# Optimization experiments

Hardware: AMD Instinct MI355X
Metric: run time of the kernel (lower is better)

## Reference

```python
import jax, jax.numpy as jnp
import numpy as np

D_MODEL = 1024
N_HEADS = 16
D_K = D_MODEL // N_HEADS
SCALE = float(np.sqrt(D_K))


def setup_inputs() -> dict:
    key = jax.random.key(0)
    ks = jax.random.split(key, 11)
    B, L, D = 2, 2048, D_MODEL
    s = 1.0 / np.sqrt(D)
    inp = {
        "q": jax.random.normal(ks[0], (B, L, D), dtype=jnp.float32),
        "k": jax.random.normal(ks[1], (B, L, D), dtype=jnp.float32),
        "v": jax.random.normal(ks[2], (B, L, D), dtype=jnp.float32),
        "Wq": jax.random.normal(ks[3], (D, D), dtype=jnp.float32) * s,
        "bq": jnp.zeros((D,), dtype=jnp.float32),
        "Wk": jax.random.normal(ks[4], (D, D), dtype=jnp.float32) * s,
        "bk": jnp.zeros((D,), dtype=jnp.float32),
        "Wv": jax.random.normal(ks[5], (D, D), dtype=jnp.float32) * s,
        "bv": jnp.zeros((D,), dtype=jnp.float32),
        "Wo": jax.random.normal(ks[6], (D, D), dtype=jnp.float32) * s,
        "bo": jnp.zeros((D,), dtype=jnp.float32),
    }
    return inp


def reference(q, k, v, Wq, bq, Wk, bk, Wv, bv, Wo, bo):
    B, L, D = q.shape
    H, Dk = N_HEADS, D_K
    # projections: [B,L,D] -> [B,H,L,Dk]
    def proj(x, W, b):
        y = x @ W + b
        return y.reshape(B, -1, H, Dk).transpose(0, 2, 1, 3)
    qh = proj(q, Wq, bq)
    kh = proj(k, Wk, bk)
    vh = proj(v, Wv, bv)
    # scores [B,H,Lq,Lk]
    scores = jnp.einsum("bhqd,bhkd->bhqk", qh, kh) / SCALE
    attn = jax.nn.softmax(scores, axis=-1)  # dropout=0.0 -> identity
    out = jnp.einsum("bhqk,bhkd->bhqd", attn, vh)
    out = out.transpose(0, 2, 1, 3).reshape(B, -1, D)
    return out @ Wo + bo
```

## Files before the change

### kernel.cpp

```cpp
#include <hip/hip_runtime.h>
#include <hip/hip_bf16.h>
#include <stdint.h>
#include <stddef.h>

typedef unsigned short ushortT;
typedef __attribute__((ext_vector_type(8))) short bf16x8s;
typedef __attribute__((ext_vector_type(4))) float f32x4;


__device__ __forceinline__ short f2bf(float f) {
  unsigned u = __float_as_uint(f);
  u += 0x7FFFu + ((u >> 16) & 1u);
  return (short)(u >> 16);
}

__device__ __forceinline__ bf16x8s cvt8(const float* src) {
  const float4* p = (const float4*)src;
  float4 a = p[0], b = p[1];
  bf16x8s r;
  r[0] = f2bf(a.x); r[1] = f2bf(a.y); r[2] = f2bf(a.z); r[3] = f2bf(a.w);
  r[4] = f2bf(b.x); r[5] = f2bf(b.y); r[6] = f2bf(b.z); r[7] = f2bf(b.w);
  return r;
}

__device__ __forceinline__ void load_lds16(const ushortT* g, ushortT* l) {
  __builtin_amdgcn_global_load_lds(
      (const __attribute__((address_space(1))) void*)(g),
      (__attribute__((address_space(3))) void*)(l), 16, 0, 0);
}

__global__ __launch_bounds__(256)
void prep(const float* __restrict__ q, const float* __restrict__ k,
          const float* __restrict__ v,
          const float* __restrict__ Wq, const float* __restrict__ Wk,
          const float* __restrict__ Wv, const float* __restrict__ Wo,
          ushortT* __restrict__ Qc, ushortT* __restrict__ Kc,
          ushortT* __restrict__ Vc, ushortT* __restrict__ Wt)
{
  const int z = blockIdx.z;
  if (z < 4) {
    if (blockIdx.x >= 1024) return;
    __shared__ __align__(16) ushortT t[32][33];
    const float* W = (z == 0) ? Wq : (z == 1) ? Wk : (z == 2) ? Wv : Wo;
    ushortT* dst = Wt + (size_t)z * 1024 * 1024;
    const int x = (blockIdx.x & 31) * 32, y = (blockIdx.x >> 5) * 32;
    const int tx = threadIdx.x & 31, ty = threadIdx.x >> 5;
#pragma unroll
    for (int i = ty; i < 32; i += 8)
      t[i][tx] = (ushortT)f2bf(W[(size_t)(y + i) * 1024 + x + tx]);
    __syncthreads();
#pragma unroll
    for (int i = ty; i < 32; i += 8)
      dst[(size_t)(x + i) * 1024 + y + tx] = t[tx][i];
  } else {
    const float* src = (z == 4) ? q : (z == 5) ? k : v;
    ushortT* dst = (z == 4) ? Qc : (z == 5) ? Kc : Vc;
    const size_t i8 = ((size_t)blockIdx.x * 256 + threadIdx.x) * 8;
    *(bf16x8s*)(dst + i8) = cvt8(src + i8);
  }
}

__device__ __forceinline__ void gemm_core_128(
    const ushortT* __restrict__ A, const ushortT* __restrict__ Bt,
    int K, ushortT* As, ushortT* Bs, f32x4 (&acc)[4][4], int m0, int n0)
{
  const int tid  = threadIdx.x;
  const int wave = tid >> 6, lane = tid & 63;
  const int wm = (wave & 1) << 6;
  const int wn = (wave >> 1) << 6;
  const int lr = lane & 15;
  const int lk = (lane >> 4) << 3;

#pragma unroll
  for (int mi = 0; mi < 4; ++mi)
#pragma unroll
    for (int ni = 0; ni < 4; ++ni)
      acc[mi][ni] = (f32x4){0.f, 0.f, 0.f, 0.f};

  for (int k0 = 0; k0 < K; k0 += 32) {
    __syncthreads();
#pragma unroll
    for (int i = 0; i < 2; ++i) {
      const int cc  = tid + (i << 8);
      const int row = cc >> 2;
      const int ko  = (cc & 3) << 3;
      load_lds16(A  + (size_t)(m0 + row) * K + k0 + ko, As + cc * 8);
      load_lds16(Bt + (size_t)(n0 + row) * K + k0 + ko, Bs + cc * 8);
    }
    __syncthreads();

    bf16x8s af[4], bfr[4];
#pragma unroll
    for (int i = 0; i < 4; ++i)
      af[i] = *(const bf16x8s*)(As + (wm + i * 16 + lr) * 32 + lk);
#pragma unroll
    for (int i = 0; i < 4; ++i)
      bfr[i] = *(const bf16x8s*)(Bs + (wn + i * 16 + lr) * 32 + lk);

#pragma unroll
    for (int mi = 0; mi < 4; ++mi)
#pragma unroll
      for (int ni = 0; ni < 4; ++ni)
        acc[mi][ni] = __builtin_amdgcn_mfma_f32_16x16x32_bf16(
            af[mi], bfr[ni], acc[mi][ni], 0, 0, 0);
  }
}

__global__ __launch_bounds__(256)
void proj_gemm(const ushortT* __restrict__ Qc, const ushortT* __restrict__ Kc,
               const ushortT* __restrict__ Vc, const ushortT* __restrict__ WtAll,
               const float* __restrict__ bq, const float* __restrict__ bk,
               const float* __restrict__ bv,
               ushortT* __restrict__ Qh, ushortT* __restrict__ Kh,
               ushortT* __restrict__ Vt)
{
  __shared__ __align__(16) ushortT As[128 * 32];
  __shared__ __align__(16) ushortT Bs[128 * 32];
  const int which = blockIdx.z;
  const ushortT* A  = (which == 0) ? Qc : (which == 1) ? Kc : Vc;
  const ushortT* Bt = WtAll + (size_t)which * 1024 * 1024;
  const float* bias = (which == 0) ? bq : (which == 1) ? bk : bv;
  const int m0 = blockIdx.x * 128, n0 = blockIdx.y * 128;

  f32x4 acc[4][4];
  gemm_core_128(A, Bt, 1024, As, Bs, acc, m0, n0);

  const int lane = threadIdx.x & 63, wave = threadIdx.x >> 6;
  const int wm = (wave & 1) << 6, wn = (wave >> 1) << 6;
  const int lr = lane & 15, quad = lane >> 4;
  const float QSCALE = 0.18033688011112042f;

#pragma unroll
  for (int ni = 0; ni < 4; ++ni) {
    const int n = n0 + wn + ni * 16 + lr;
    const float bias_v = bias[n];
    const int h = n >> 6, d = n & 63;
#pragma unroll
    for (int mi = 0; mi < 4; ++mi) {
#pragma unroll
      for (int r = 0; r < 4; ++r) {
        const int m = m0 + wm + mi * 16 + quad * 4 + r;
        const int b = m >> 11, l = m & 2047;
        float val = acc[mi][ni][r] + bias_v;
        if (which == 0) val *= QSCALE;
        const ushortT o = (ushortT)f2bf(val);
        const size_t bh = (size_t)(b * 16 + h);
        if (which == 0)      Qh[(bh * 2048 + l) * 64 + d] = o;
        else if (which == 1) Kh[(bh * 2048 + l) * 64 + d] = o;
        else                 Vt[(bh * 64 + d) * 2048 + l] = o;
      }
    }
  }
}

__global__ __launch_bounds__(256)
void attn_kernel(const ushortT* __restrict__ Qh, const ushortT* __restrict__ Kh,
                 const ushortT* __restrict__ Vt, ushortT* __restrict__ Ob)
{
  const int b = blockIdx.z, h = blockIdx.y, qt = blockIdx.x;
  const int bh = b * 16 + h;
  const int wave = threadIdx.x >> 6, lane = threadIdx.x & 63;
  const int lr = lane & 15, quad = lane >> 4, lk = quad * 8;
  const int q0 = qt * 128 + wave * 32;

  const ushortT* Q = Qh + ((size_t)bh * 2048 + q0) * 64;
  const ushortT* K = Kh + (size_t)bh * 2048 * 64;
  const ushortT* V = Vt + (size_t)bh * 64 * 2048;

  __shared__ __align__(16) ushortT Ks[64 * 76];
  __shared__ __align__(16) ushortT Vs[64 * 76];
  __shared__ __align__(16) ushortT P4[4][32 * 76];
  ushortT* Pw = P4[wave];

  bf16x8s qf[2][2];
#pragma unroll
  for (int mt = 0; mt < 2; ++mt) {
    qf[mt][0] = *(const bf16x8s*)(Q + (mt * 16 + lr) * 64 + lk);
    qf[mt][1] = *(const bf16x8s*)(Q + (mt * 16 + lr) * 64 + 32 + lk);
  }

  f32x4 o[2][4];
#pragma unroll
  for (int mt = 0; mt < 2; ++mt)
#pragma unroll
    for (int nt = 0; nt < 4; ++nt) o[mt][nt] = (f32x4){0.f, 0.f, 0.f, 0.f};
  float lsum[2][4] = {{0.f, 0.f, 0.f, 0.f}, {0.f, 0.f, 0.f, 0.f}};

  const int tid = threadIdx.x;
  const int srow = tid >> 3;
  const int sc8  = (tid & 7) << 3;

  bf16x8s kch[2], vch[2];
#pragma unroll
  for (int i = 0; i < 2; ++i) {
    const int row = srow + i * 32;
    kch[i] = *(const bf16x8s*)(K + (size_t)row * 64 + sc8);
    vch[i] = *(const bf16x8s*)(V + (size_t)row * 2048 + sc8);
  }

  for (int kt = 0; kt < 2048; kt += 64) {
    __syncthreads();
#pragma unroll
    for (int i = 0; i < 2; ++i) {
      const int row = srow + i * 32;
      *(bf16x8s*)(Ks + row * 76 + sc8) = kch[i];
      *(bf16x8s*)(Vs + row * 76 + sc8) = vch[i];
    }
    __syncthreads();

    const int kn = (kt + 64) & 2047;
#pragma unroll
    for (int i = 0; i < 2; ++i) {
      const int row = srow + i * 32;
      kch[i] = *(const bf16x8s*)(K + (size_t)(kn + row) * 64 + sc8);
      vch[i] = *(const bf16x8s*)(V + (size_t)row * 2048 + kn + sc8);
    }

    f32x4 s[2][4];
#pragma unroll
    for (int mt = 0; mt < 2; ++mt)
#pragma unroll
      for (int t = 0; t < 4; ++t) s[mt][t] = (f32x4){0.f, 0.f, 0.f, 0.f};
#pragma unroll
    for (int t = 0; t < 4; ++t) {
      const bf16x8s kf0 = *(const bf16x8s*)(Ks + (t * 16 + lr) * 76 + lk);
      const bf16x8s kf1 = *(const bf16x8s*)(Ks + (t * 16 + lr) * 76 + 32 + lk);
#pragma unroll
      for (int mt = 0; mt < 2; ++mt) {
        s[mt][t] = __builtin_amdgcn_mfma_f32_16x16x32_bf16(qf[mt][0], kf0, s[mt][t], 0, 0, 0);
        s[mt][t] = __builtin_amdgcn_mfma_f32_16x16x32_bf16(qf[mt][1], kf1, s[mt][t], 0, 0, 0);
      }
    }

#pragma unroll
    for (int mt = 0; mt < 2; ++mt)
#pragma unroll
      for (int t = 0; t < 4; ++t)
#pragma unroll
        for (int r = 0; r < 4; ++r) {
          const float p = __builtin_amdgcn_exp2f(s[mt][t][r]);
          lsum[mt][r] += p;
          Pw[(mt * 16 + quad * 4 + r) * 76 + t * 16 + lr] = (ushortT)f2bf(p);
        }
    asm volatile("s_waitcnt lgkmcnt(0)" ::: "memory");

    bf16x8s pf[2][2];
#pragma unroll
    for (int mt = 0; mt < 2; ++mt) {
      pf[mt][0] = *(const bf16x8s*)(Pw + (mt * 16 + lr) * 76 + lk);
      pf[mt][1] = *(const bf16x8s*)(Pw + (mt * 16 + lr) * 76 + 32 + lk);
    }
#pragma unroll
    for (int nt = 0; nt < 4; ++nt) {
      const bf16x8s vf0 = *(const bf16x8s*)(Vs + (nt * 16 + lr) * 76 + lk);
      const bf16x8s vf1 = *(const bf16x8s*)(Vs + (nt * 16 + lr) * 76 + 32 + lk);
#pragma unroll
      for (int mt = 0; mt < 2; ++mt) {
        o[mt][nt] = __builtin_amdgcn_mfma_f32_16x16x32_bf16(pf[mt][0], vf0, o[mt][nt], 0, 0, 0);
        o[mt][nt] = __builtin_amdgcn_mfma_f32_16x16x32_bf16(pf[mt][1], vf1, o[mt][nt], 0, 0, 0);
      }
    }
  }

  float inv[2][4];
#pragma unroll
  for (int mt = 0; mt < 2; ++mt)
#pragma unroll
    for (int r = 0; r < 4; ++r) {
      float s = lsum[mt][r];
      s += __shfl_xor(s, 1);
      s += __shfl_xor(s, 2);
      s += __shfl_xor(s, 4);
      s += __shfl_xor(s, 8);
      inv[mt][r] = 1.0f / s;
    }
#pragma unroll
  for (int mt = 0; mt < 2; ++mt)
#pragma unroll
    for (int nt = 0; nt < 4; ++nt) {
      const int dcol = h * 64 + nt * 16 + lr;
#pragma unroll
      for (int r = 0; r < 4; ++r) {
        const int l = q0 + mt * 16 + quad * 4 + r;
        Ob[((size_t)b * 2048 + l) * 1024 + dcol] =
            (ushortT)f2bf(o[mt][nt][r] * inv[mt][r]);
      }
    }
}

__global__ __launch_bounds__(256)
void out_gemm(const ushortT* __restrict__ Ob, const ushortT* __restrict__ Wto,
              const float* __restrict__ bo, float* __restrict__ C)
{
  __shared__ __align__(16) ushortT As[128 * 32];
  __shared__ __align__(16) ushortT Bs[128 * 32];
  const int m0 = blockIdx.x * 128, n0 = blockIdx.y * 128;

  f32x4 acc[4][4];
  gemm_core_128(Ob, Wto, 1024, As, Bs, acc, m0, n0);

  const int lane = threadIdx.x & 63, wave = threadIdx.x >> 6;
  const int wm = (wave & 1) << 6, wn = (wave >> 1) << 6;
  const int lr = lane & 15, quad = lane >> 4;

#pragma unroll
  for (int ni = 0; ni < 4; ++ni) {
    const int n = n0 + wn + ni * 16 + lr;
    const float bias_v = bo[n];
#pragma unroll
    for (int mi = 0; mi < 4; ++mi) {
#pragma unroll
      for (int r = 0; r < 4; ++r) {
        const int m = m0 + wm + mi * 16 + quad * 4 + r;
        C[(size_t)m * 1024 + n] = acc[mi][ni][r] + bias_v;
      }
    }
  }
}

extern "C" void kernel_launch(void* const* d_in, const int* in_sizes, int n_in,
                              void* d_out, int out_size, void* d_ws, size_t ws_size,
                              hipStream_t stream) {
  const float* q  = (const float*)d_in[0];
  const float* k  = (const float*)d_in[1];
  const float* v  = (const float*)d_in[2];
  const float* Wq = (const float*)d_in[3];
  const float* bq = (const float*)d_in[4];
  const float* Wk = (const float*)d_in[5];
  const float* bk = (const float*)d_in[6];
  const float* Wv = (const float*)d_in[7];
  const float* bv = (const float*)d_in[8];
  const float* Wo = (const float*)d_in[9];
  const float* bo = (const float*)d_in[10];

  char* ws = (char*)d_ws;
  ushortT* Wt = (ushortT*)(ws);
  ushortT* Qh = (ushortT*)(ws + (size_t)(8  << 20));
  ushortT* Kh = (ushortT*)(ws + (size_t)(16 << 20));
  ushortT* Vt = (ushortT*)(ws + (size_t)(24 << 20));
  ushortT* Qc = (ushortT*)(ws + (size_t)(32 << 20));
  ushortT* Kc = (ushortT*)(ws + (size_t)(40 << 20));
  ushortT* Vc = (ushortT*)(ws + (size_t)(48 << 20));
  ushortT* Ob = Qc;

  prep<<<dim3(2048, 1, 7), 256, 0, stream>>>(q, k, v, Wq, Wk, Wv, Wo,
                                             Qc, Kc, Vc, Wt);
  proj_gemm<<<dim3(32, 8, 3), 256, 0, stream>>>(Qc, Kc, Vc, Wt, bq, bk, bv,
                                                Qh, Kh, Vt);
  attn_kernel<<<dim3(16, 16, 2), 256, 0, stream>>>(Qh, Kh, Vt, Ob);
  out_gemm<<<dim3(32, 8), 256, 0, stream>>>(Ob, Wt + (size_t)3 * 1024 * 1024,
                                            bo, (float*)d_out);
}
```

Baseline: 265.6 us.

## Transpose score MFMA so exp results pack into vectorized P stores

```diff
diff --git a/kernel.cpp b/kernel.cpp
--- a/kernel.cpp
+++ b/kernel.cpp
@@ -169,7 +169,7 @@
 
   __shared__ __align__(16) ushortT Ks[64 * 76];
   __shared__ __align__(16) ushortT Vs[64 * 76];
-  __shared__ __align__(16) ushortT P4[4][32 * 76];
+  __shared__ __align__(16) ushortT P4[4][32 * 88];
   ushortT* Pw = P4[wave];
 
   bf16x8s qf[2][2];
@@ -184,21 +184,20 @@
   for (int mt = 0; mt < 2; ++mt)
 #pragma unroll
     for (int nt = 0; nt < 4; ++nt) o[mt][nt] = (f32x4){0.f, 0.f, 0.f, 0.f};
-  float lsum[2][4] = {{0.f, 0.f, 0.f, 0.f}, {0.f, 0.f, 0.f, 0.f}};
+  float lsum[2] = {0.f, 0.f};
 
   const int tid = threadIdx.x;
   const int srow = tid >> 3;
   const int sc8  = (tid & 7) << 3;
 
-  bf16x8s kch[2], vch[2];
-#pragma unroll
-  for (int i = 0; i < 2; ++i) {
-    const int row = srow + i * 32;
-    kch[i] = *(const bf16x8s*)(K + (size_t)row * 64 + sc8);
-    vch[i] = *(const bf16x8s*)(V + (size_t)row * 2048 + sc8);
-  }
-
   for (int kt = 0; kt < 2048; kt += 64) {
+    bf16x8s kch[2], vch[2];
+#pragma unroll
+    for (int i = 0; i < 2; ++i) {
+      const int row = srow + i * 32;
+      kch[i] = *(const bf16x8s*)(K + (size_t)(kt + row) * 64 + sc8);
+      vch[i] = *(const bf16x8s*)(V + (size_t)row * 2048 + kt + sc8);
+    }
     __syncthreads();
 #pragma unroll
     for (int i = 0; i < 2; ++i) {
@@ -208,14 +207,6 @@
     }
     __syncthreads();
 
-    const int kn = (kt + 64) & 2047;
-#pragma unroll
-    for (int i = 0; i < 2; ++i) {
-      const int row = srow + i * 32;
-      kch[i] = *(const bf16x8s*)(K + (size_t)(kn + row) * 64 + sc8);
-      vch[i] = *(const bf16x8s*)(V + (size_t)row * 2048 + kn + sc8);
-    }
-
     f32x4 s[2][4];
 #pragma unroll
     for (int mt = 0; mt < 2; ++mt)
@@ -227,28 +218,36 @@
       const bf16x8s kf1 = *(const bf16x8s*)(Ks + (t * 16 + lr) * 76 + 32 + lk);
 #pragma unroll
       for (int mt = 0; mt < 2; ++mt) {
-        s[mt][t] = __builtin_amdgcn_mfma_f32_16x16x32_bf16(qf[mt][0], kf0, s[mt][t], 0, 0, 0);
-        s[mt][t] = __builtin_amdgcn_mfma_f32_16x16x32_bf16(qf[mt][1], kf1, s[mt][t], 0, 0, 0);
+        s[mt][t] = __builtin_amdgcn_mfma_f32_16x16x32_bf16(kf0, qf[mt][0], s[mt][t], 0, 0, 0);
+        s[mt][t] = __builtin_amdgcn_mfma_f32_16x16x32_bf16(kf1, qf[mt][1], s[mt][t], 0, 0, 0);
       }
     }
 
 #pragma unroll
     for (int mt = 0; mt < 2; ++mt)
 #pragma unroll
-      for (int t = 0; t < 4; ++t)
-#pragma unroll
-        for (int r = 0; r < 4; ++r) {
-          const float p = __builtin_amdgcn_exp2f(s[mt][t][r]);
-          lsum[mt][r] += p;
-          Pw[(mt * 16 + quad * 4 + r) * 76 + t * 16 + lr] = (ushortT)f2bf(p);
-        }
+      for (int t = 0; t < 4; ++t) {
+        const float e0 = __builtin_amdgcn_exp2f(s[mt][t][0]);
+        const float e1 = __builtin_amdgcn_exp2f(s[mt][t][1]);
+        const float e2 = __builtin_amdgcn_exp2f(s[mt][t][2]);
+        const float e3 = __builtin_amdgcn_exp2f(s[mt][t][3]);
+        lsum[mt] += (e0 + e1) + (e2 + e3);
+        const unsigned a0 = __float_as_uint(e0) + 0x8000u;
+        const unsigned a1 = __float_as_uint(e1) + 0x8000u;
+        const unsigned a2 = __float_as_uint(e2) + 0x8000u;
+        const unsigned a3 = __float_as_uint(e3) + 0x8000u;
+        uint2 d;
+        d.x = (a0 >> 16) | (a1 & 0xFFFF0000u);
+        d.y = (a2 >> 16) | (a3 & 0xFFFF0000u);
+        *(uint2*)(Pw + (mt * 16 + lr) * 88 + t * 16 + quad * 4) = d;
+      }
     asm volatile("s_waitcnt lgkmcnt(0)" ::: "memory");
 
     bf16x8s pf[2][2];
 #pragma unroll
     for (int mt = 0; mt < 2; ++mt) {
-      pf[mt][0] = *(const bf16x8s*)(Pw + (mt * 16 + lr) * 76 + lk);
-      pf[mt][1] = *(const bf16x8s*)(Pw + (mt * 16 + lr) * 76 + 32 + lk);
+      pf[mt][0] = *(const bf16x8s*)(Pw + (mt * 16 + lr) * 88 + lk);
+      pf[mt][1] = *(const bf16x8s*)(Pw + (mt * 16 + lr) * 88 + 32 + lk);
     }
 #pragma unroll
     for (int nt = 0; nt < 4; ++nt) {
@@ -262,18 +261,21 @@
     }
   }
 
-  float inv[2][4];
+  float* fP = (float*)Pw;
+#pragma unroll
+  for (int mt = 0; mt < 2; ++mt) {
+    float s = lsum[mt];
+    s += __shfl_xor(s, 16);
+    s += __shfl_xor(s, 32);
+    fP[mt * 16 + lr] = 1.0f / s;
+  }
+  asm volatile("s_waitcnt lgkmcnt(0)" ::: "memory");
+  float invr[2][4];
 #pragma unroll
   for (int mt = 0; mt < 2; ++mt)
 #pragma unroll
-    for (int r = 0; r < 4; ++r) {
-      float s = lsum[mt][r];
-      s += __shfl_xor(s, 1);
-      s += __shfl_xor(s, 2);
-      s += __shfl_xor(s, 4);
-      s += __shfl_xor(s, 8);
-      inv[mt][r] = 1.0f / s;
-    }
+    for (int r = 0; r < 4; ++r) invr[mt][r] = fP[mt * 16 + quad * 4 + r];
+
 #pragma unroll
   for (int mt = 0; mt < 2; ++mt)
 #pragma unroll
@@ -283,7 +285,7 @@
       for (int r = 0; r < 4; ++r) {
         const int l = q0 + mt * 16 + quad * 4 + r;
         Ob[((size_t)b * 2048 + l) * 1024 + dcol] =
-            (ushortT)f2bf(o[mt][nt][r] * inv[mt][r]);
+            (ushortT)f2bf(o[mt][nt][r] * invr[mt][r]);
       }
     }
 }
```

New measurement: 239.4 us. 9.9% less time.
